# Optimization experiments

Hardware: AMD Instinct MI355X
Metric: run time of the kernel (lower is better)

The kernel has to match this reference:

```python
import jax, jax.numpy as jnp
import numpy as np

N = 10000      # nodes
E = 100000     # edges
C = 32         # in_channels == hidden_channels == out_channels
ED = 4         # edge_dim
G = 64         # number of graphs in the batch
EPS = 1e-5     # BatchNorm eps


def setup_inputs() -> dict:
    key = jax.random.key(0)
    ks = jax.random.split(key, 20)
    rn = lambda k, shape, s=0.05: jax.random.normal(k, shape, dtype=jnp.float32) * s
    return {
        "x": jax.random.normal(ks[0], (N, C), dtype=jnp.float32),
        "edge_attr": jax.random.normal(ks[1], (E, ED), dtype=jnp.float32),
        # edge MLP 1: ED -> C -> C*C ; NNConv1 root/bias
        "e1_w1": rn(ks[2], (ED, C)), "e1_b1": jnp.zeros((C,), jnp.float32),
        "e1_w2": rn(ks[3], (C, C * C)), "e1_b2": jnp.zeros((C * C,), jnp.float32),
        "root1": rn(ks[4], (C, C)), "bias1": jnp.zeros((C,), jnp.float32),
        # edge MLP 2: ED -> C -> C*C ; NNConv2 root/bias
        "e2_w1": rn(ks[5], (ED, C)), "e2_b1": jnp.zeros((C,), jnp.float32),
        "e2_w2": rn(ks[6], (C, C * C)), "e2_b2": jnp.zeros((C * C,), jnp.float32),
        "root2": rn(ks[7], (C, C)), "bias2": jnp.zeros((C,), jnp.float32),
        # BatchNorm (eval mode: running stats)
        "bn1_g": jnp.ones((C,), jnp.float32), "bn1_b": jnp.zeros((C,), jnp.float32),
        "bn1_m": rn(ks[8], (C,), 0.1), "bn1_v": 1.0 + 0.1 * jax.random.uniform(ks[9], (C,), dtype=jnp.float32),
        "bn2_g": jnp.ones((C,), jnp.float32), "bn2_b": jnp.zeros((C,), jnp.float32),
        "bn2_m": rn(ks[10], (C,), 0.1), "bn2_v": 1.0 + 0.1 * jax.random.uniform(ks[11], (C,), dtype=jnp.float32),
        # readout: C -> C//2 -> 1
        "r1_w": rn(ks[12], (C, C // 2)), "r1_b": jnp.zeros((C // 2,), jnp.float32),
        "r2_w": rn(ks[13], (C // 2, 1)), "r2_b": jnp.zeros((1,), jnp.float32),
        "edge_index": jax.random.randint(ks[14], (2, E), 0, N),
        "batch": jnp.sort(jax.random.randint(ks[15], (N,), 0, G)),
    }


def _nnconv(x, edge_index, edge_attr, w1, b1, w2, b2, root, bias):
    # edge MLP -> per-edge weight matrix [E, C, C]
    h = jax.nn.relu(edge_attr @ w1 + b1)
    W = (h @ w2 + b2).reshape(E, C, C)
    src, dst = edge_index[0], edge_index[1]
    # gather source features, per-edge matmul, scatter-mean to target nodes
    msg = jnp.einsum('ei,eio->eo', x[src], W)                      # [E, C]
    agg = jax.ops.segment_sum(msg, dst, num_segments=N)            # [N, C]
    cnt = jax.ops.segment_sum(jnp.ones((E,), x.dtype), dst, num_segments=N)
    agg = agg / jnp.maximum(cnt, 1.0)[:, None]
    return agg + x @ root + bias


def _bn(x, g, b, m, v):
    return (x - m) * jax.lax.rsqrt(v + EPS) * g + b


def reference(x, edge_attr,
              e1_w1, e1_b1, e1_w2, e1_b2, root1, bias1,
              e2_w1, e2_b1, e2_w2, e2_b2, root2, bias2,
              bn1_g, bn1_b, bn1_m, bn1_v,
              bn2_g, bn2_b, bn2_m, bn2_v,
              r1_w, r1_b, r2_w, r2_b,
              edge_index, batch):
    h = jax.nn.relu(_bn(_nnconv(x, edge_index, edge_attr, e1_w1, e1_b1, e1_w2, e1_b2, root1, bias1),
                        bn1_g, bn1_b, bn1_m, bn1_v))
    h = jax.nn.relu(_bn(_nnconv(h, edge_index, edge_attr, e2_w1, e2_b1, e2_w2, e2_b2, root2, bias2),
                        bn2_g, bn2_b, bn2_m, bn2_v))
    # global mean pool over graphs
    psum = jax.ops.segment_sum(h, batch, num_segments=G)           # [G, C]
    pcnt = jax.ops.segment_sum(jnp.ones((N,), h.dtype), batch, num_segments=G)
    pooled = psum / jnp.maximum(pcnt, 1.0)[:, None]
    # readout MLP (dropout is identity in eval)
    return jax.nn.relu(pooled @ r1_w + r1_b) @ r2_w + r2_b          # [G, 1]
```

## Files before the change

### kernel.cpp

```cpp
#include <hip/hip_runtime.h>

#define NN 10000
#define EE 100000
#define CC 32
#define GG 64
#define EPSV 1e-5f
#define NB 8
#define SLOTS 1056
#define PST 36
#define PNODE (32*PST)
#define HBLK ((EE+255)/256)
#define WBLK 160

__global__ __launch_bounds__(256) void k_pre(const int* __restrict__ ei,
        int* __restrict__ cnt, int* __restrict__ deg,
        const float* __restrict__ w2a, const float* __restrict__ b2a,
        const float* __restrict__ w2b, const float* __restrict__ b2b,
        float* __restrict__ w2r1, float* __restrict__ w2r2) {
    int blk = blockIdx.x;
    int t = threadIdx.x;
    if (blk < HBLK) {
        int e = blk * 256 + t;
        if (e < EE) {
            atomicAdd(&cnt[ei[EE + e]], 1);
            atomicAdd(&deg[ei[e]], 1);
        }
    } else {
        int b2i = blk - HBLK;
        int s = (b2i % 5) * 256 + t;
        int i = b2i / 5;
        if (s < SLOTS) {
            float va = (s < 1024) ? w2a[(s >> 5) * 1024 + i * 32 + (s & 31)]
                                  : b2a[i * 32 + (s - 1024)];
            float vb = (s < 1024) ? w2b[(s >> 5) * 1024 + i * 32 + (s & 31)]
                                  : b2b[i * 32 + (s - 1024)];
            w2r1[i * SLOTS + s] = va;
            w2r2[i * SLOTS + s] = vb;
        }
    }
}

__global__ __launch_bounds__(1024) void k_scan(const int* __restrict__ deg,
                                               const int* __restrict__ cnt,
                                               int* __restrict__ rowptr,
                                               int* __restrict__ cursor,
                                               int* __restrict__ colptr,
                                               int* __restrict__ ccursor) {
    __shared__ int buf[1024];
    int t = threadIdx.x;
    int base = t * 10;
    for (int pass = 0; pass < 2; pass++) {
        const int* src = pass ? cnt : deg;
        int* dst_p = pass ? colptr : rowptr;
        int* dst_c = pass ? ccursor : cursor;
        int v[10]; int s = 0;
        #pragma unroll
        for (int k = 0; k < 10; k++) {
            int idx = base + k;
            v[k] = (idx < NN) ? src[idx] : 0;
            s += v[k];
        }
        buf[t] = s;
        for (int off = 1; off < 1024; off <<= 1) {
            __syncthreads();
            int val = buf[t] + ((t >= off) ? buf[t - off] : 0);
            __syncthreads();
            buf[t] = val;
        }
        __syncthreads();
        int carry = (t > 0) ? buf[t - 1] : 0;
        #pragma unroll
        for (int k = 0; k < 10; k++) {
            int idx = base + k;
            if (idx < NN) { dst_p[idx] = carry; dst_c[idx] = carry; }
            carry += v[k];
        }
        if (t == 1023) dst_p[NN] = buf[1023];
        __syncthreads();
    }
}

__global__ void k_scatter(const int* __restrict__ ei,
        const float* __restrict__ edge_attr,
        int* __restrict__ cursor, int* __restrict__ ccursor,
        int* __restrict__ msrc, int* __restrict__ cpos,
        float4* __restrict__ ea_csr) {
    int e = blockIdx.x * 256 + threadIdx.x;
    if (e >= EE) return;
    int sn = ei[e];
    int dn = ei[EE + e];
    float4 a = *(const float4*)&edge_attr[(size_t)e * 4];
    int pos = atomicAdd(&cursor[sn], 1);
    msrc[pos] = sn;
    ea_csr[pos] = a;
    int cp = atomicAdd(&ccursor[dn], 1);
    cpos[cp] = pos;
}

__global__ __launch_bounds__(256, 3) void k_fused3(const float* __restrict__ x,
        const float4* __restrict__ ea_csr,
        const float* __restrict__ w1, const float* __restrict__ b1,
        const float* __restrict__ w2r,
        const int* __restrict__ msrc, const int* __restrict__ rowptr,
        float* __restrict__ msg) {
    __shared__ float xs[NB][32];
    __shared__ float P2[NB * PNODE];
    __shared__ float shx[8][32];
    int t = threadIdx.x;
    int o = t & 31;
    int cb = 4 * (t >> 5);
    int n0 = blockIdx.x * NB;

    int ebase = rowptr[n0];
    int eend  = rowptr[n0 + NB];
    int grp = t >> 5;

    float wc0 = w1[o], wc1 = w1[32 + o], wc2 = w1[64 + o], wc3 = w1[96 + o];
    float bb  = b1[o];

    int pos = ebase + grp;
    float4 aC = make_float4(0.f, 0.f, 0.f, 0.f);
    int srcC = n0;
    if (pos < eend) {
        aC = ea_csr[pos];
        srcC = msrc[pos];
    }

    xs[t >> 5][t & 31] = x[n0 * 32 + t];
    __syncthreads();

    {
        float acc[4][NB];
        #pragma unroll
        for (int k = 0; k < 4; k++)
            #pragma unroll
            for (int n = 0; n < NB; n++) acc[k][n] = 0.f;
        #pragma unroll
        for (int j = 0; j < 8; j++) {
            float wk[4][4];
            #pragma unroll
            for (int r = 0; r < 4; r++)
                #pragma unroll
                for (int k = 0; k < 4; k++)
                    wk[r][k] = w2r[(4 * j + r) * SLOTS + (cb + k) * 32 + o];
            #pragma unroll
            for (int n = 0; n < NB; n++) {
                float4 xq = *(const float4*)&xs[n][4 * j];
                #pragma unroll
                for (int k = 0; k < 4; k++)
                    acc[k][n] += xq.x * wk[0][k] + xq.y * wk[1][k]
                               + xq.z * wk[2][k] + xq.w * wk[3][k];
            }
        }
        #pragma unroll
        for (int n = 0; n < NB; n++) {
            float4 st = make_float4(acc[0][n], acc[1][n], acc[2][n], acc[3][n]);
            *(float4*)&P2[n * PNODE + o * PST + cb] = st;
        }
    }
    if (t < 32) {
        float wb[32];
        #pragma unroll
        for (int i = 0; i < 32; i++) wb[i] = w2r[i * SLOTS + 1024 + t];
        #pragma unroll
        for (int n = 0; n < NB; n++) {
            float b = 0.f;
            #pragma unroll
            for (int j = 0; j < 8; j++) {
                float4 xq = *(const float4*)&xs[n][4 * j];
                b += xq.x * wb[4 * j] + xq.y * wb[4 * j + 1]
                   + xq.z * wb[4 * j + 2] + xq.w * wb[4 * j + 3];
            }
            *(float4*)&P2[n * PNODE + t * PST + 32] = make_float4(b, 0.f, 0.f, 0.f);
        }
    }
    __syncthreads();

    while (pos < eend) {
        int pn = pos + 8;
        float4 aN = aC; int srcN = srcC;
        if (pn < eend) {
            aN = ea_csr[pn];
            srcN = msrc[pn];
        }
        float h = fmaxf(aC.x * wc0 + aC.y * wc1 + aC.z * wc2 + aC.w * wc3 + bb, 0.f);
        shx[grp][o] = h;
        asm volatile("" ::: "memory");
        const float* Pn = &P2[(srcC - n0) * PNODE + o * PST];
        float m = Pn[32];
        #pragma unroll
        for (int b = 0; b < 8; b++) {
            float4 hx = *(const float4*)&shx[grp][4 * b];
            float4 pq = *(const float4*)&Pn[4 * b];
            m += hx.x * pq.x + hx.y * pq.y + hx.z * pq.z + hx.w * pq.w;
        }
        msg[(size_t)pos * 32 + o] = m;
        asm volatile("" ::: "memory");
        pos = pn; aC = aN; srcC = srcN;
    }
}

__global__ __launch_bounds__(256) void k_combine(const float* __restrict__ x_in,
        const float* __restrict__ msg,
        const int* __restrict__ colptr, const int* __restrict__ cpos,
        const float* __restrict__ root, const float* __restrict__ bias,
        const float* __restrict__ bng, const float* __restrict__ bnb,
        const float* __restrict__ bnm, const float* __restrict__ bnv,
        float* __restrict__ x_out, float* __restrict__ psum,
        const int* __restrict__ batch) {
    __shared__ float xs[8][32];
    __shared__ float vals[8][32];
    __shared__ int gb[8];
    int t = threadIdx.x;
    int n0 = blockIdx.x * 8;
    xs[t >> 5][t & 31] = x_in[n0 * 32 + t];
    __syncthreads();
    int k = t >> 5, o = t & 31, n = n0 + k;
    float r = bias[o];
    #pragma unroll
    for (int i = 0; i < 32; i++) r += xs[k][i] * root[i * 32 + o];
    int jbase = colptr[n], jend = colptr[n + 1];
    float acc = 0.f;
    for (int jb = jbase; jb < jend; jb += 32) {
        int nrem = jend - jb;
        int lim = (nrem < 32) ? nrem : 32;
        int cv = 0;
        if (o < lim) cv = cpos[jb + o];
        for (int j = 0; j < lim; j += 8) {
            float v[8];
            #pragma unroll
            for (int q = 0; q < 8; q++) {
                if (j + q < lim) {
                    int cj = __shfl(cv, j + q, 32);
                    v[q] = msg[(size_t)cj * 32 + o];
                } else v[q] = 0.f;
            }
            #pragma unroll
            for (int q = 0; q < 8; q++) acc += v[q];
        }
    }
    float a = acc / fmaxf((float)(jend - jbase), 1.f);
    float val = a + r;
    val = (val - bnm[o]) * rsqrtf(bnv[o] + EPSV) * bng[o] + bnb[o];
    val = fmaxf(val, 0.f);
    if (x_out) {
        x_out[(size_t)n * 32 + o] = val;
    }
    if (psum) {
        vals[k][o] = val;
        if (o == 0) gb[k] = batch[n];
        __syncthreads();
        if (k == 0) {
            float pacc = vals[0][o];
            int g = gb[0];
            #pragma unroll
            for (int k2 = 1; k2 < 8; k2++) {
                if (gb[k2] == g) pacc += vals[k2][o];
                else {
                    atomicAdd(&psum[(size_t)g * 32 + o], pacc);
                    g = gb[k2]; pacc = vals[k2][o];
                }
            }
            atomicAdd(&psum[(size_t)g * 32 + o], pacc);
        }
    }
}

__global__ __launch_bounds__(256) void k_readout(const float* __restrict__ psum,
        const int* __restrict__ batch,
        const float* __restrict__ r1w, const float* __restrict__ r1b,
        const float* __restrict__ r2w, const float* __restrict__ r2b,
        float* __restrict__ out) {
    __shared__ float w1s[32 * 16];
    __shared__ float b1s[16];
    __shared__ float w2s[16];
    __shared__ float ps[GG * 32];
    int t = threadIdx.x;
    int cnt_g = 0;
    if (t < GG) {
        int lo = 0, hi = NN;
        while (lo < hi) { int m = (lo + hi) >> 1; if (batch[m] < t) lo = m + 1; else hi = m; }
        int lb = lo;
        lo = 0; hi = NN;
        while (lo < hi) { int m = (lo + hi) >> 1; if (batch[m] < t + 1) lo = m + 1; else hi = m; }
        cnt_g = lo - lb;
    }
    w1s[t] = r1w[t];
    w1s[t + 256] = r1w[t + 256];
    if (t < 16) { b1s[t] = r1b[t]; w2s[t] = r2w[t]; }
    #pragma unroll
    for (int i = 0; i < GG * 32 / 256; i++) ps[t + i * 256] = psum[t + i * 256];
    __syncthreads();
    if (t < GG) {
        float inv = 1.f / fmaxf((float)cnt_g, 1.f);
        float acc = r2b[0];
        #pragma unroll
        for (int j = 0; j < 16; j++) {
            float dot = 0.f;
            #pragma unroll
            for (int c = 0; c < 32; c++) dot += ps[t * 32 + c] * w1s[c * 16 + j];
            float z = dot * inv + b1s[j];
            acc += fmaxf(z, 0.f) * w2s[j];
        }
        out[t] = acc;
    }
}

extern "C" void kernel_launch(void* const* d_in, const int* in_sizes, int n_in,
                              void* d_out, int out_size, void* d_ws, size_t ws_size,
                              hipStream_t stream) {
    const float* x       = (const float*)d_in[0];
    const float* eattr   = (const float*)d_in[1];
    const float* e1_w1   = (const float*)d_in[2];
    const float* e1_b1   = (const float*)d_in[3];
    const float* e1_w2   = (const float*)d_in[4];
    const float* e1_b2   = (const float*)d_in[5];
    const float* root1   = (const float*)d_in[6];
    const float* bias1   = (const float*)d_in[7];
    const float* e2_w1   = (const float*)d_in[8];
    const float* e2_b1   = (const float*)d_in[9];
    const float* e2_w2   = (const float*)d_in[10];
    const float* e2_b2   = (const float*)d_in[11];
    const float* root2   = (const float*)d_in[12];
    const float* bias2   = (const float*)d_in[13];
    const float* bn1_g   = (const float*)d_in[14];
    const float* bn1_b   = (const float*)d_in[15];
    const float* bn1_m   = (const float*)d_in[16];
    const float* bn1_v   = (const float*)d_in[17];
    const float* bn2_g   = (const float*)d_in[18];
    const float* bn2_b   = (const float*)d_in[19];
    const float* bn2_m   = (const float*)d_in[20];
    const float* bn2_v   = (const float*)d_in[21];
    const float* r1_w    = (const float*)d_in[22];
    const float* r1_b    = (const float*)d_in[23];
    const float* r2_w    = (const float*)d_in[24];
    const float* r2_b    = (const float*)d_in[25];
    const int*   ei      = (const int*)d_in[26];
    const int*   batch   = (const int*)d_in[27];

    char* ws = (char*)d_ws;
    float*  w2r1   = (float*) (ws);
    float*  w2r2   = (float*) (ws + 135168);
    float*  msg    = (float*) (ws + 270336);
    float4* ea_csr = (float4*)(ws + 13070336);
    int*    cnt    = (int*)   (ws + 14670336);
    int*    deg    = (int*)   (ws + 14710336);
    float*  psum   = (float*) (ws + 14750336);
    float*  xmid   = (float*) (ws + 14758528);
    int*    rowptr = (int*)   (ws + 16038528);
    int*    cursor = (int*)   (ws + 16078592);
    int*    colptr = (int*)   (ws + 16118592);
    int*    ccursor= (int*)   (ws + 16158656);
    int*    msrc   = (int*)   (ws + 16198656);
    int*    cpos   = (int*)   (ws + 16598656);

    hipMemsetAsync(ws + 14670336, 0, 88192, stream);

    k_pre<<<HBLK + WBLK, 256, 0, stream>>>(ei, cnt, deg,
                                           e1_w2, e1_b2, e2_w2, e2_b2, w2r1, w2r2);
    k_scan<<<1, 1024, 0, stream>>>(deg, cnt, rowptr, cursor, colptr, ccursor);
    k_scatter<<<(EE + 255) / 256, 256, 0, stream>>>(ei, eattr,
                                                    cursor, ccursor, msrc, cpos,
                                                    ea_csr);

    k_fused3<<<NN / NB, 256, 0, stream>>>(x, ea_csr, e1_w1, e1_b1, w2r1,
                                          msrc, rowptr, msg);
    k_combine<<<NN / 8, 256, 0, stream>>>(x, msg, colptr, cpos, root1, bias1,
                                          bn1_g, bn1_b, bn1_m, bn1_v,
                                          xmid, nullptr, batch);

    k_fused3<<<NN / NB, 256, 0, stream>>>(xmid, ea_csr, e2_w1, e2_b1, w2r2,
                                          msrc, rowptr, msg);
    k_combine<<<NN / 8, 256, 0, stream>>>(xmid, msg, colptr, cpos, root2, bias2,
                                          bn2_g, bn2_b, bn2_m, bn2_v,
                                          nullptr, psum, batch);

    k_readout<<<1, 256, 0, stream>>>(psum, batch, r1_w, r1_b, r2_w, r2_b, (float*)d_out);
}
```

Before: 255.0 us.

## Fuse layer-1 combine with layer-2 messages, fold readout via last-block, parallelize scan

Fuses the first layer's combine/BN/ReLU step into the second layer's message kernel, so each block computes its 8 nodes' xmid and immediately builds the per-node projection tiles. It uses a separate msg2 buffer so the fused kernel can read msg1 while writing msg2. The readout kernel is folded into the final combine through a last-block-done atomic counter. The two prefix scans now run as two separate blocks instead of sequentially in one. The aim is to cut kernel launches and a serial single-block tail, at the cost of a larger workspace and a threadfence/atomic in every block of the final kernel.

```diff
diff --git a/kernel.cpp b/kernel.cpp
--- a/kernel.cpp
+++ b/kernel.cpp
@@ -2,15 +2,31 @@
 
 #define NN 10000
 #define EE 100000
-#define CC 32
 #define GG 64
 #define EPSV 1e-5f
-#define NB 8
 #define SLOTS 1056
 #define PST 36
 #define PNODE (32*PST)
-#define HBLK ((EE+255)/256)
+#define HBLK 391
 #define WBLK 160
+#define NBK 1250
+
+#define OFF_W2R1   0
+#define OFF_W2R2   135168
+#define OFF_MSG1   270336
+#define OFF_MSG2   13070336
+#define OFF_EACSR  25870336
+#define OFF_CNT    27470336
+#define OFF_DEG    27510336
+#define OFF_PSUM   27550336
+#define OFF_DONE   27558528
+#define OFF_XMID   27558592
+#define OFF_ROWPTR 28838592
+#define OFF_CURSOR 28878656
+#define OFF_COLPTR 28918656
+#define OFF_CCUR   28958720
+#define OFF_MSRC   28998720
+#define OFF_CPOS   29398720
 
 __global__ __launch_bounds__(256) void k_pre(const int* __restrict__ ei,
         int* __restrict__ cnt, int* __restrict__ deg,
@@ -40,44 +56,42 @@
     }
 }
 
-__global__ __launch_bounds__(1024) void k_scan(const int* __restrict__ deg,
-                                               const int* __restrict__ cnt,
-                                               int* __restrict__ rowptr,
-                                               int* __restrict__ cursor,
-                                               int* __restrict__ colptr,
-                                               int* __restrict__ ccursor) {
+__global__ __launch_bounds__(1024) void k_scan2(const int* __restrict__ deg,
+                                                const int* __restrict__ cnt,
+                                                int* __restrict__ rowptr,
+                                                int* __restrict__ cursor,
+                                                int* __restrict__ colptr,
+                                                int* __restrict__ ccursor) {
     __shared__ int buf[1024];
+    int pass = blockIdx.x;
+    const int* src = pass ? cnt : deg;
+    int* dst_p = pass ? colptr : rowptr;
+    int* dst_c = pass ? ccursor : cursor;
     int t = threadIdx.x;
     int base = t * 10;
-    for (int pass = 0; pass < 2; pass++) {
-        const int* src = pass ? cnt : deg;
-        int* dst_p = pass ? colptr : rowptr;
-        int* dst_c = pass ? ccursor : cursor;
-        int v[10]; int s = 0;
-        #pragma unroll
-        for (int k = 0; k < 10; k++) {
-            int idx = base + k;
-            v[k] = (idx < NN) ? src[idx] : 0;
-            s += v[k];
-        }
-        buf[t] = s;
-        for (int off = 1; off < 1024; off <<= 1) {
-            __syncthreads();
-            int val = buf[t] + ((t >= off) ? buf[t - off] : 0);
-            __syncthreads();
-            buf[t] = val;
-        }
+    int v[10]; int s = 0;
+    #pragma unroll
+    for (int k = 0; k < 10; k++) {
+        int idx = base + k;
+        v[k] = (idx < NN) ? src[idx] : 0;
+        s += v[k];
+    }
+    buf[t] = s;
+    for (int off = 1; off < 1024; off <<= 1) {
         __syncthreads();
-        int carry = (t > 0) ? buf[t - 1] : 0;
-        #pragma unroll
-        for (int k = 0; k < 10; k++) {
-            int idx = base + k;
-            if (idx < NN) { dst_p[idx] = carry; dst_c[idx] = carry; }
-            carry += v[k];
-        }
-        if (t == 1023) dst_p[NN] = buf[1023];
+        int val = buf[t] + ((t >= off) ? buf[t - off] : 0);
         __syncthreads();
-    }
+        buf[t] = val;
+    }
+    __syncthreads();
+    int carry = (t > 0) ? buf[t - 1] : 0;
+    #pragma unroll
+    for (int k = 0; k < 10; k++) {
+        int idx = base + k;
+        if (idx < NN) { dst_p[idx] = carry; dst_c[idx] = carry; }
+        carry += v[k];
+    }
+    if (t == 1023) dst_p[NN] = buf[1023];
 }
 
 __global__ void k_scatter(const int* __restrict__ ei,
@@ -97,22 +111,22 @@
     cpos[cp] = pos;
 }
 
-__global__ __launch_bounds__(256, 3) void k_fused3(const float* __restrict__ x,
+__global__ __launch_bounds__(256, 3) void k_f1(const float* __restrict__ x,
         const float4* __restrict__ ea_csr,
         const float* __restrict__ w1, const float* __restrict__ b1,
         const float* __restrict__ w2r,
         const int* __restrict__ msrc, const int* __restrict__ rowptr,
         float* __restrict__ msg) {
-    __shared__ float xs[NB][32];
-    __shared__ float P2[NB * PNODE];
+    __shared__ float xs[8][32];
+    __shared__ float P2[8 * PNODE];
     __shared__ float shx[8][32];
     int t = threadIdx.x;
     int o = t & 31;
     int cb = 4 * (t >> 5);
-    int n0 = blockIdx.x * NB;
+    int n0 = blockIdx.x * 8;
 
     int ebase = rowptr[n0];
-    int eend  = rowptr[n0 + NB];
+    int eend  = rowptr[n0 + 8];
     int grp = t >> 5;
 
     float wc0 = w1[o], wc1 = w1[32 + o], wc2 = w1[64 + o], wc3 = w1[96 + o];
@@ -121,20 +135,17 @@
     int pos = ebase + grp;
     float4 aC = make_float4(0.f, 0.f, 0.f, 0.f);
     int srcC = n0;
-    if (pos < eend) {
-        aC = ea_csr[pos];
-        srcC = msrc[pos];
-    }
-
-    xs[t >> 5][t & 31] = x[n0 * 32 + t];
+    if (pos < eend) { aC = ea_csr[pos]; srcC = msrc[pos]; }
+
+    xs[grp][o] = x[n0 * 32 + t];
     __syncthreads();
 
     {
-        float acc[4][NB];
+        float acc[4][8];
         #pragma unroll
         for (int k = 0; k < 4; k++)
             #pragma unroll
-            for (int n = 0; n < NB; n++) acc[k][n] = 0.f;
+            for (int n = 0; n < 8; n++) acc[k][n] = 0.f;
         #pragma unroll
         for (int j = 0; j < 8; j++) {
             float wk[4][4];
@@ -144,7 +155,7 @@
                 for (int k = 0; k < 4; k++)
                     wk[r][k] = w2r[(4 * j + r) * SLOTS + (cb + k) * 32 + o];
             #pragma unroll
-            for (int n = 0; n < NB; n++) {
+            for (int n = 0; n < 8; n++) {
                 float4 xq = *(const float4*)&xs[n][4 * j];
                 #pragma unroll
                 for (int k = 0; k < 4; k++)
@@ -153,7 +164,7 @@
             }
         }
         #pragma unroll
-        for (int n = 0; n < NB; n++) {
+        for (int n = 0; n < 8; n++) {
             float4 st = make_float4(acc[0][n], acc[1][n], acc[2][n], acc[3][n]);
             *(float4*)&P2[n * PNODE + o * PST + cb] = st;
         }
@@ -163,7 +174,7 @@
         #pragma unroll
         for (int i = 0; i < 32; i++) wb[i] = w2r[i * SLOTS + 1024 + t];
         #pragma unroll
-        for (int n = 0; n < NB; n++) {
+        for (int n = 0; n < 8; n++) {
             float b = 0.f;
             #pragma unroll
             for (int j = 0; j < 8; j++) {
@@ -179,10 +190,7 @@
     while (pos < eend) {
         int pn = pos + 8;
         float4 aN = aC; int srcN = srcC;
-        if (pn < eend) {
-            aN = ea_csr[pn];
-            srcN = msrc[pn];
-        }
+        if (pn < eend) { aN = ea_csr[pn]; srcN = msrc[pn]; }
         float h = fmaxf(aC.x * wc0 + aC.y * wc1 + aC.z * wc2 + aC.w * wc3 + bb, 0.f);
         shx[grp][o] = h;
         asm volatile("" ::: "memory");
@@ -200,25 +208,168 @@
     }
 }
 
-__global__ __launch_bounds__(256) void k_combine(const float* __restrict__ x_in,
-        const float* __restrict__ msg,
+__global__ __launch_bounds__(256, 3) void k_mid(const float* __restrict__ x,
+        const float* __restrict__ msg1,
         const int* __restrict__ colptr, const int* __restrict__ cpos,
-        const float* __restrict__ root, const float* __restrict__ bias,
-        const float* __restrict__ bng, const float* __restrict__ bnb,
-        const float* __restrict__ bnm, const float* __restrict__ bnv,
-        float* __restrict__ x_out, float* __restrict__ psum,
-        const int* __restrict__ batch) {
+        const float* __restrict__ root1, const float* __restrict__ bias1,
+        const float* __restrict__ bn1g, const float* __restrict__ bn1b,
+        const float* __restrict__ bn1m, const float* __restrict__ bn1v,
+        const float4* __restrict__ ea_csr,
+        const float* __restrict__ w1, const float* __restrict__ b1,
+        const float* __restrict__ w2r,
+        const int* __restrict__ msrc, const int* __restrict__ rowptr,
+        float* __restrict__ xmid, float* __restrict__ msg2) {
+    __shared__ float xs[8][32];
+    __shared__ float P2[8 * PNODE];
+    __shared__ float shx[8][32];
+    __shared__ float xmid_s[8][32];
+    int t = threadIdx.x;
+    int o = t & 31;
+    int grp = t >> 5;
+    int cb = 4 * grp;
+    int n0 = blockIdx.x * 8;
+
+    int ebase = rowptr[n0];
+    int eend  = rowptr[n0 + 8];
+
+    float wc0 = w1[o], wc1 = w1[32 + o], wc2 = w1[64 + o], wc3 = w1[96 + o];
+    float hbb = b1[o];
+    int pos = ebase + grp;
+    float4 aC = make_float4(0.f, 0.f, 0.f, 0.f);
+    int srcC = n0;
+    if (pos < eend) { aC = ea_csr[pos]; srcC = msrc[pos]; }
+
+    xs[grp][o] = x[n0 * 32 + t];
+    __syncthreads();
+    {
+        int k = grp, n = n0 + k;
+        float rt = bias1[o];
+        #pragma unroll
+        for (int i = 0; i < 32; i++) rt += xs[k][i] * root1[i * 32 + o];
+        int jbase = colptr[n], jend = colptr[n + 1];
+        float acc = 0.f;
+        for (int jb = jbase; jb < jend; jb += 32) {
+            int nrem = jend - jb;
+            int lim = (nrem < 32) ? nrem : 32;
+            int cv = 0;
+            if (o < lim) cv = cpos[jb + o];
+            for (int j = 0; j < lim; j += 8) {
+                float v[8];
+                #pragma unroll
+                for (int q = 0; q < 8; q++) {
+                    if (j + q < lim) {
+                        int cj = __shfl(cv, j + q, 32);
+                        v[q] = msg1[(size_t)cj * 32 + o];
+                    } else v[q] = 0.f;
+                }
+                #pragma unroll
+                for (int q = 0; q < 8; q++) acc += v[q];
+            }
+        }
+        float a = acc / fmaxf((float)(jend - jbase), 1.f);
+        float val = a + rt;
+        val = (val - bn1m[o]) * rsqrtf(bn1v[o] + EPSV) * bn1g[o] + bn1b[o];
+        val = fmaxf(val, 0.f);
+        xmid_s[k][o] = val;
+        xmid[(size_t)n * 32 + o] = val;
+    }
+    __syncthreads();
+
+    {
+        float acc[4][8];
+        #pragma unroll
+        for (int k = 0; k < 4; k++)
+            #pragma unroll
+            for (int n = 0; n < 8; n++) acc[k][n] = 0.f;
+        #pragma unroll
+        for (int j = 0; j < 8; j++) {
+            float wk[4][4];
+            #pragma unroll
+            for (int r = 0; r < 4; r++)
+                #pragma unroll
+                for (int k = 0; k < 4; k++)
+                    wk[r][k] = w2r[(4 * j + r) * SLOTS + (cb + k) * 32 + o];
+            #pragma unroll
+            for (int n = 0; n < 8; n++) {
+                float4 xq = *(const float4*)&xmid_s[n][4 * j];
+                #pragma unroll
+                for (int k = 0; k < 4; k++)
+                    acc[k][n] += xq.x * wk[0][k] + xq.y * wk[1][k]
+                               + xq.z * wk[2][k] + xq.w * wk[3][k];
+            }
+        }
+        #pragma unroll
+        for (int n = 0; n < 8; n++) {
+            float4 st = make_float4(acc[0][n], acc[1][n], acc[2][n], acc[3][n]);
+            *(float4*)&P2[n * PNODE + o * PST + cb] = st;
+        }
+    }
+    if (t < 32) {
+        float wb[32];
+        #pragma unroll
+        for (int i = 0; i < 32; i++) wb[i] = w2r[i * SLOTS + 1024 + t];
+        #pragma unroll
+        for (int n = 0; n < 8; n++) {
+            float b = 0.f;
+            #pragma unroll
+            for (int j = 0; j < 8; j++) {
+                float4 xq = *(const float4*)&xmid_s[n][4 * j];
+                b += xq.x * wb[4 * j] + xq.y * wb[4 * j + 1]
+                   + xq.z * wb[4 * j + 2] + xq.w * wb[4 * j + 3];
+            }
+            *(float4*)&P2[n * PNODE + t * PST + 32] = make_float4(b, 0.f, 0.f, 0.f);
+        }
+    }
+    __syncthreads();
+
+    while (pos < eend) {
+        int pn = pos + 8;
+        float4 aN = aC; int srcN = srcC;
+        if (pn < eend) { aN = ea_csr[pn]; srcN = msrc[pn]; }
+        float h = fmaxf(aC.x * wc0 + aC.y * wc1 + aC.z * wc2 + aC.w * wc3 + hbb, 0.f);
+        shx[grp][o] = h;
+        asm volatile("" ::: "memory");
+        const float* Pn = &P2[(srcC - n0) * PNODE + o * PST];
+        float m = Pn[32];
+        #pragma unroll
+        for (int b = 0; b < 8; b++) {
+            float4 hx = *(const float4*)&shx[grp][4 * b];
+            float4 pq = *(const float4*)&Pn[4 * b];
+            m += hx.x * pq.x + hx.y * pq.y + hx.z * pq.z + hx.w * pq.w;
+        }
+        msg2[(size_t)pos * 32 + o] = m;
+        asm volatile("" ::: "memory");
+        pos = pn; aC = aN; srcC = srcN;
+    }
+}
+
+__global__ __launch_bounds__(256) void k_end(const float* __restrict__ xmid,
+        const float* __restrict__ msg2,
+        const int* __restrict__ colptr, const int* __restrict__ cpos,
+        const float* __restrict__ root2, const float* __restrict__ bias2,
+        const float* __restrict__ bn2g, const float* __restrict__ bn2b,
+        const float* __restrict__ bn2m, const float* __restrict__ bn2v,
+        const int* __restrict__ batch, float* __restrict__ psum,
+        int* __restrict__ done,
+        const float* __restrict__ r1w, const float* __restrict__ r1b,
+        const float* __restrict__ r2w, const float* __restrict__ r2b,
+        float* __restrict__ out) {
     __shared__ float xs[8][32];
     __shared__ float vals[8][32];
     __shared__ int gb[8];
+    __shared__ float rd[2592];
+    __shared__ int lastflag;
     int t = threadIdx.x;
+    int o = t & 31;
+    int grp = t >> 5;
     int n0 = blockIdx.x * 8;
-    xs[t >> 5][t & 31] = x_in[n0 * 32 + t];
-    __syncthreads();
-    int k = t >> 5, o = t & 31, n = n0 + k;
-    float r = bias[o];
+
+    xs[grp][o] = xmid[(size_t)n0 * 32 + t];
+    __syncthreads();
+    int k = grp, n = n0 + k;
+    float rt = bias2[o];
     #pragma unroll
-    for (int i = 0; i < 32; i++) r += xs[k][i] * root[i * 32 + o];
+    for (int i = 0; i < 32; i++) rt += xs[k][i] * root2[i * 32 + o];
     int jbase = colptr[n], jend = colptr[n + 1];
     float acc = 0.f;
     for (int jb = jbase; jb < jend; jb += 32) {
@@ -232,7 +383,7 @@
             for (int q = 0; q < 8; q++) {
                 if (j + q < lim) {
                     int cj = __shfl(cv, j + q, 32);
-                    v[q] = msg[(size_t)cj * 32 + o];
+                    v[q] = msg2[(size_t)cj * 32 + o];
                 } else v[q] = 0.f;
             }
             #pragma unroll
@@ -240,69 +391,69 @@
         }
     }
     float a = acc / fmaxf((float)(jend - jbase), 1.f);
-    float val = a + r;
-    val = (val - bnm[o]) * rsqrtf(bnv[o] + EPSV) * bng[o] + bnb[o];
+    float val = a + rt;
+    val = (val - bn2m[o]) * rsqrtf(bn2v[o] + EPSV) * bn2g[o] + bn2b[o];
     val = fmaxf(val, 0.f);
-    if (x_out) {
-        x_out[(size_t)n * 32 + o] = val;
-    }
-    if (psum) {
-        vals[k][o] = val;
-        if (o == 0) gb[k] = batch[n];
-        __syncthreads();
-        if (k == 0) {
-            float pacc = vals[0][o];
-            int g = gb[0];
-            #pragma unroll
-            for (int k2 = 1; k2 < 8; k2++) {
-                if (gb[k2] == g) pacc += vals[k2][o];
-                else {
-                    atomicAdd(&psum[(size_t)g * 32 + o], pacc);
-                    g = gb[k2]; pacc = vals[k2][o];
-                }
-            }
-            atomicAdd(&psum[(size_t)g * 32 + o], pacc);
-        }
-    }
-}
-
-__global__ __launch_bounds__(256) void k_readout(const float* __restrict__ psum,
-        const int* __restrict__ batch,
-        const float* __restrict__ r1w, const float* __restrict__ r1b,
-        const float* __restrict__ r2w, const float* __restrict__ r2b,
-        float* __restrict__ out) {
-    __shared__ float w1s[32 * 16];
-    __shared__ float b1s[16];
-    __shared__ float w2s[16];
-    __shared__ float ps[GG * 32];
-    int t = threadIdx.x;
+    vals[k][o] = val;
+    if (o == 0) gb[k] = batch[n];
+    __syncthreads();
+    if (k == 0) {
+        float pacc = vals[0][o];
+        int g = gb[0];
+        #pragma unroll
+        for (int k2 = 1; k2 < 8; k2++) {
+            if (gb[k2] == g) pacc += vals[k2][o];
+            else {
+                atomicAdd(&psum[(size_t)g * 32 + o], pacc);
+                g = gb[k2]; pacc = vals[k2][o];
+            }
+        }
+        atomicAdd(&psum[(size_t)g * 32 + o], pacc);
+    }
+    __syncthreads();
+
+    if (t == 0) {
+        __threadfence();
+        int old = atomicAdd(done, 1);
+        lastflag = (old == NBK - 1);
+    }
+    __syncthreads();
+    if (!lastflag) return;
+    __threadfence();
+
+    float* w1s = rd;
+    float* b1s = rd + 512;
+    float* w2s = rd + 528;
+    float* ps  = rd + 544;
     int cnt_g = 0;
     if (t < GG) {
         int lo = 0, hi = NN;
-        while (lo < hi) { int m = (lo + hi) >> 1; if (batch[m] < t) lo = m + 1; else hi = m; }
+        while (lo < hi) { int m2 = (lo + hi) >> 1; if (batch[m2] < t) lo = m2 + 1; else hi = m2; }
         int lb = lo;
         lo = 0; hi = NN;
-        while (lo < hi) { int m = (lo + hi) >> 1; if (batch[m] < t + 1) lo = m + 1; else hi = m; }
+        while (lo < hi) { int m2 = (lo + hi) >> 1; if (batch[m2] < t + 1) lo = m2 + 1; else hi = m2; }
         cnt_g = lo - lb;
     }
     w1s[t] = r1w[t];
     w1s[t + 256] = r1w[t + 256];
     if (t < 16) { b1s[t] = r1b[t]; w2s[t] = r2w[t]; }
     #pragma unroll
-    for (int i = 0; i < GG * 32 / 256; i++) ps[t + i * 256] = psum[t + i * 256];
+    for (int i = 0; i < GG * 32 / 256; i++)
+        ps[t + i * 256] = __hip_atomic_load(&psum[t + i * 256], __ATOMIC_RELAXED,
+                                            __HIP_MEMORY_SCOPE_AGENT);
     __syncthreads();
     if (t < GG) {
         float inv = 1.f / fmaxf((float)cnt_g, 1.f);
-        float acc = r2b[0];
+        float acc2 = r2b[0];
         #pragma unroll
         for (int j = 0; j < 16; j++) {
             float dot = 0.f;
             #pragma unroll
             for (int c = 0; c < 32; c++) dot += ps[t * 32 + c] * w1s[c * 16 + j];
             float z = dot * inv + b1s[j];
-            acc += fmaxf(z, 0.f) * w2s[j];
-        }
-        out[t] = acc;
+            acc2 += fmaxf(z, 0.f) * w2s[j];
+        }
+        out[t] = acc2;
     }
 }
 
@@ -339,41 +490,40 @@
     const int*   batch   = (const int*)d_in[27];
 
     char* ws = (char*)d_ws;
-    float*  w2r1   = (float*) (ws);
-    float*  w2r2   = (float*) (ws + 135168);
-    float*  msg    = (float*) (ws + 270336);
-    float4* ea_csr = (float4*)(ws + 13070336);
-    int*    cnt    = (int*)   (ws + 14670336);
-    int*    deg    = (int*)   (ws + 14710336);
-    float*  psum   = (float*) (ws + 14750336);
-    float*  xmid   = (float*) (ws + 14758528);
-    int*    rowptr = (int*)   (ws + 16038528);
-    int*    cursor = (int*)   (ws + 16078592);
-    int*    colptr = (int*)   (ws + 16118592);
-    int*    ccursor= (int*)   (ws + 16158656);
-    int*    msrc   = (int*)   (ws + 16198656);
-    int*    cpos   = (int*)   (ws + 16598656);
-
-    hipMemsetAsync(ws + 14670336, 0, 88192, stream);
+    float*  w2r1   = (float*) (ws + OFF_W2R1);
+    float*  w2r2   = (float*) (ws + OFF_W2R2);
+    float*  msg1   = (float*) (ws + OFF_MSG1);
+    float*  msg2   = (float*) (ws + OFF_MSG2);
+    float4* ea_csr = (float4*)(ws + OFF_EACSR);
+    int*    cnt    = (int*)   (ws + OFF_CNT);
+    int*    deg    = (int*)   (ws + OFF_DEG);
+    float*  psum   = (float*) (ws + OFF_PSUM);
+    int*    done   = (int*)   (ws + OFF_DONE);
+    float*  xmid   = (float*) (ws + OFF_XMID);
+    int*    rowptr = (int*)   (ws + OFF_ROWPTR);
+    int*    cursor = (int*)   (ws + OFF_CURSOR);
+    int*    colptr = (int*)   (ws + OFF_COLPTR);
+    int*    ccursor= (int*)   (ws + OFF_CCUR);
+    int*    msrc   = (int*)   (ws + OFF_MSRC);
+    int*    cpos   = (int*)   (ws + OFF_CPOS);
+
+    hipMemsetAsync(ws + OFF_CNT, 0, 88256, stream);
 
     k_pre<<<HBLK + WBLK, 256, 0, stream>>>(ei, cnt, deg,
                                            e1_w2, e1_b2, e2_w2, e2_b2, w2r1, w2r2);
-    k_scan<<<1, 1024, 0, stream>>>(deg, cnt, rowptr, cursor, colptr, ccursor);
+    k_scan2<<<2, 1024, 0, stream>>>(deg, cnt, rowptr, cursor, colptr, ccursor);
     k_scatter<<<(EE + 255) / 256, 256, 0, stream>>>(ei, eattr,
                                                     cursor, ccursor, msrc, cpos,
                                                     ea_csr);
 
-    k_fused3<<<NN / NB, 256, 0, stream>>>(x, ea_csr, e1_w1, e1_b1, w2r1,
-                                          msrc, rowptr, msg);
-    k_combine<<<NN / 8, 256, 0, stream>>>(x, msg, colptr, cpos, root1, bias1,
-                                          bn1_g, bn1_b, bn1_m, bn1_v,
-                                          xmid, nullptr, batch);
-
-    k_fused3<<<NN / NB, 256, 0, stream>>>(xmid, ea_csr, e2_w1, e2_b1, w2r2,
-                                          msrc, rowptr, msg);
-    k_combine<<<NN / 8, 256, 0, stream>>>(xmid, msg, colptr, cpos, root2, bias2,
-                                          bn2_g, bn2_b, bn2_m, bn2_v,
-                                          nullptr, psum, batch);
-
-    k_readout<<<1, 256, 0, stream>>>(psum, batch, r1_w, r1_b, r2_w, r2_b, (float*)d_out);
-}
+    k_f1<<<NBK, 256, 0, stream>>>(x, ea_csr, e1_w1, e1_b1, w2r1,
+                                  msrc, rowptr, msg1);
+    k_mid<<<NBK, 256, 0, stream>>>(x, msg1, colptr, cpos, root1, bias1,
+                                   bn1_g, bn1_b, bn1_m, bn1_v,
+                                   ea_csr, e2_w1, e2_b1, w2r2,
+                                   msrc, rowptr, xmid, msg2);
+    k_end<<<NBK, 256, 0, stream>>>(xmid, msg2, colptr, cpos, root2, bias2,
+                                   bn2_g, bn2_b, bn2_m, bn2_v,
+                                   batch, psum, done,
+                                   r1_w, r1_b, r2_w, r2_b, (float*)d_out);
+}
```

Measured after the change: 263.2 us. +3.2%, slower.
